# Optimization experiments

Hardware: AMD Instinct MI355X
Metric: run time of the kernel (lower is better)

## Reference

```python
import jax, jax.numpy as jnp
import numpy as np

B, N, C = 1, 768, 128


def _safe_cdist(x):
    # Euclidean pairwise distance, grad-safe at zero (diagonal).
    sq = jnp.sum(x * x, axis=-1)  # (b, n)
    d2 = sq[:, :, None] + sq[:, None, :] - 2.0 * jnp.einsum('bmi,bni->bmn', x, x)
    d2 = jnp.maximum(d2, 0.0)
    pos = d2 > 0
    return jnp.where(pos, jnp.sqrt(jnp.where(pos, d2, 1.0)), 0.0)


def _bilinear(h, Wa, ba, Wb, bb):
    # Gated bilinear unit: Linear_a(h) * Linear_b(h)
    return (h @ Wa.T + ba) * (h @ Wb.T + bb)


def setup_inputs() -> dict:
    key = jax.random.key(0)
    ks = jax.random.split(key, 16)
    x = jax.random.normal(ks[0], (B, N, 3), dtype=jnp.float32)

    def lin(k, fan_in, fan_out):
        k1, k2 = jax.random.split(k)
        s = 1.0 / np.sqrt(fan_in)
        W = jax.random.uniform(k1, (fan_out, fan_in), jnp.float32, -s, s)
        b = jax.random.uniform(k2, (fan_out,), jnp.float32, -s, s)
        return W, b

    Wa1, ba1 = lin(ks[1], 3, C)
    Wb1, bb1 = lin(ks[2], 3, C)
    Wa2, ba2 = lin(ks[3], C, C)
    Wb2, bb2 = lin(ks[4], C, C)
    Wa3, ba3 = lin(ks[5], C, C)
    Wb3, bb3 = lin(ks[6], C, C)
    Wf, _ = lin(ks[7], C, 2)  # final bias unused by the einsum in forward
    return {"x": x,
            "Wa1": Wa1, "ba1": ba1, "Wb1": Wb1, "bb1": bb1,
            "Wa2": Wa2, "ba2": ba2, "Wb2": Wb2, "bb2": bb2,
            "Wa3": Wa3, "ba3": ba3, "Wb3": Wb3, "bb3": bb3,
            "Wf": Wf}


def reference(x, Wa1, ba1, Wb1, bb1, Wa2, ba2, Wb2, bb2, Wa3, ba3, Wb3, bb3, Wf):
    b, n, _ = x.shape
    nrm = jnp.linalg.norm(x, axis=-1, keepdims=True)          # (b, n, 1)
    nrm_m = jnp.broadcast_to(nrm, (b, n, n))                  # row norms
    d = _safe_cdist(x)                                        # (b, n, n)
    h = jnp.stack([d, nrm_m, jnp.swapaxes(nrm_m, 1, 2)], axis=-1)  # (b,n,n,3)
    h = _bilinear(h, Wa1, ba1, Wb1, bb1)
    h = _bilinear(h, Wa2, ba2, Wb2, bb2)
    h = _bilinear(h, Wa3, ba3, Wb3, bb3)                      # (b,n,n,C)
    att = jax.nn.softmax(h, axis=-2)                          # softmax over n (dim=-2)
    # einsum('bmnc,bni->bmic') followed by sum over m, fused:
    agg = jnp.einsum('bmnc,bni->bic', att, x)                 # (b, 3, C)
    agg = jnp.swapaxes(agg, 1, 2)                             # (b, C, 3)
    out = jnp.einsum('bnd,on->bod', agg, Wf)                  # (b, 2, 3)
    return jnp.concatenate([x[:, :1], out[:, :2]], axis=1)    # (b, 3, 3)
```

## Files before the change

### kernel.cpp

```cpp
#include <hip/hip_runtime.h>

#define NPTS 768
#define CCH  128
#define NM4  36
#define NM2  10
#define NCHUNK 2
#define CTILE (NPTS/NCHUNK)
#define PAIR (NPTS*CCH)
#define NACC 384
#define FINB 96
#define LOG2E 1.4426950408889634f

typedef __attribute__((ext_vector_type(8))) short bf16x8;
typedef __attribute__((ext_vector_type(16))) float f32x16;
union Frag { unsigned int u[4]; bf16x8 h; };

__device__ __forceinline__ float fast_exp2(float x) {
  return __builtin_amdgcn_exp2f(x);
}

__device__ __forceinline__ void split3(float x, unsigned int& h0,
                                       unsigned int& h1, unsigned int& h2) {
  const unsigned int b0 = __float_as_uint(x);
  h0 = b0 >> 16;
  const float r1 = x - __uint_as_float(b0 & 0xFFFF0000u);
  const unsigned int b1 = __float_as_uint(r1);
  h1 = b1 >> 16;
  const float r2 = r1 - __uint_as_float(b1 & 0xFFFF0000u);
  h2 = __float_as_uint(r2) >> 16;
}

__device__ __forceinline__ int t4i(int a, int b, int c) {
  int t = 0;
  for (int aa = 0; aa < a; ++aa) t += (5 - aa) * (6 - aa) / 2;
  for (int bb = 0; bb < b; ++bb) t += (5 - a - bb);
  return t + c;
}
__device__ __forceinline__ int t2i(int a, int b, int c) {
  int t = 0;
  for (int aa = 0; aa < a; ++aa) t += (3 - aa) * (4 - aa) / 2;
  for (int bb = 0; bb < b; ++bb) t += (3 - a - bb);
  return t + c;
}

__global__ __launch_bounds__(128) void k_fold12(
    const float* __restrict__ x,
    const float* __restrict__ Wa1, const float* __restrict__ ba1,
    const float* __restrict__ Wb1, const float* __restrict__ bb1,
    const float* __restrict__ Wa2, const float* __restrict__ ba2,
    const float* __restrict__ Wb2, const float* __restrict__ bb2,
    float* __restrict__ norms, float* __restrict__ C2m,
    float* __restrict__ apart, unsigned int* __restrict__ ticket) {
  __shared__ float sA[128][NM2];
  __shared__ float sB[128][NM2];
  const int c = blockIdx.x;
  const int k = threadIdx.x;

  if (c < 6) {
    const int i = c*128 + k;
    const float p0 = x[3*i], p1 = x[3*i+1], p2 = x[3*i+2];
    norms[i] = sqrtf(p0*p0 + p1*p1 + p2*p2);
  }
  if (c == 6) {
    apart[k] = 0.f; apart[CCH + k] = 0.f; apart[2*CCH + k] = 0.f;
    if (k == 0) *ticket = 0u;
  }

  {
    const float A0 = Wa1[3*k], A1 = Wa1[3*k+1], A2c = Wa1[3*k+2], A3 = ba1[k];
    const float B0 = Wb1[3*k], B1 = Wb1[3*k+1], B2c = Wb1[3*k+2], B3 = bb1[k];
    const float g0 = A3*B3;
    const float g1 = A2c*B3 + A3*B2c;
    const float g2 = A2c*B2c;
    const float g3 = A1*B3 + A3*B1;
    const float g4 = A1*B2c + A2c*B1;
    const float g5 = A1*B1;
    const float g6 = A0*B3 + A3*B0;
    const float g7 = A0*B2c + A2c*B0;
    const float g8 = A0*B1 + A1*B0;
    const float g9 = A0*B0;
    const float wa = Wa2[c*CCH + k];
    const float wb = Wb2[c*CCH + k];
    sA[k][0] = wa*g0; sB[k][0] = wb*g0;
    sA[k][1] = wa*g1; sB[k][1] = wb*g1;
    sA[k][2] = wa*g2; sB[k][2] = wb*g2;
    sA[k][3] = wa*g3; sB[k][3] = wb*g3;
    sA[k][4] = wa*g4; sB[k][4] = wb*g4;
    sA[k][5] = wa*g5; sB[k][5] = wb*g5;
    sA[k][6] = wa*g6; sB[k][6] = wb*g6;
    sA[k][7] = wa*g7; sB[k][7] = wb*g7;
    sA[k][8] = wa*g8; sB[k][8] = wb*g8;
    sA[k][9] = wa*g9; sB[k][9] = wb*g9;
  }
  __syncthreads();

  for (int s = 64; s >= 1; s >>= 1) {
    if (k < s) {
      for (int t = 0; t < NM2; ++t) {
        sA[k][t] += sA[k+s][t];
        sB[k][t] += sB[k+s][t];
      }
    }
    __syncthreads();
  }
  if (k == 0) {
    sA[0][0] += ba2[c];
    sB[0][0] += bb2[c];
  }
  __syncthreads();

  if (k < 35) {
    int rem = k, a = 0;
    while (rem >= (5 - a)*(6 - a)/2) { rem -= (5 - a)*(6 - a)/2; ++a; }
    int b = 0;
    while (rem >= 5 - a - b) { rem -= 5 - a - b; ++b; }
    const int cc = rem;
    float s = 0.f;
    const int deg = a + b + cc;
    for (int a1 = 0; a1 <= a && a1 <= 2; ++a1)
      for (int b1 = 0; b1 <= b && b1 <= 2; ++b1)
        for (int c1 = 0; c1 <= cc && c1 <= 2; ++c1) {
          const int d1 = a1 + b1 + c1;
          if (d1 <= 2 && (deg - d1) <= 2)
            s += sA[0][t2i(a1, b1, c1)]
               * sB[0][t2i(a - a1, b - b1, cc - c1)];
        }
    C2m[c*NM4 + k] = s;
  }
  if (k == 35) C2m[c*NM4 + 35] = 0.f;
}

__global__ void k_pre2(const float* __restrict__ Wa3, const float* __restrict__ ba3,
                       const float* __restrict__ Wb3, const float* __restrict__ bb3,
                       const float* __restrict__ C2m,
                       float* __restrict__ A3mT, float* __restrict__ B3mT) {
  const int c = blockIdx.x;
  const int j = threadIdx.x;
  if (j >= NM4) return;
  float sa = 0.f, sb = 0.f;
  if (j < 35) {
    for (int k = 0; k < CCH; ++k) {
      const float v = C2m[k*NM4 + j];
      sa += Wa3[c*CCH + k] * v;
      sb += Wb3[c*CCH + k] * v;
    }
    if (j == 0) { sa += ba3[c]; sb += bb3[c]; }
  }
  A3mT[j*CCH + c] = sa;
  B3mT[j*CCH + c] = sb;
}

__global__ __launch_bounds__(256, 4) void k_main(
    const float* __restrict__ x, const float* __restrict__ norms,
    const float* __restrict__ A3mT, const float* __restrict__ B3mT,
    float* __restrict__ Mp, float* __restrict__ Sp,
    float* __restrict__ A0p, float* __restrict__ A1p, float* __restrict__ A2p) {
  __shared__ __align__(16) float4 xt[CTILE];
  const int tid = threadIdx.x;
  const int wid = tid >> 6;
  const int lane = tid & 63;
  const int hl = lane >> 5;
  const int ln = lane & 31;
  const int m = blockIdx.x;
  const int chunk = blockIdx.y;
  const int c = wid*32 + ln;

  for (int p = tid; p < CTILE; p += 256) {
    const int n = chunk*CTILE + p;
    xt[p] = make_float4(x[3*n], x[3*n+1], x[3*n+2], norms[n]);
  }

  const float u = norms[m];
  const float xm0 = x[3*m], xm1 = x[3*m+1], xm2 = x[3*m+2];
  const float uu = u*u;
  const float up[5] = {1.f, u, uu, uu*u, uu*uu};

  Frag ba0, ba1, ba2, bb0, bb1, bb2;
  #pragma unroll
  for (int p = 0; p < 4; ++p) {
    unsigned int wa0 = 0, wa1 = 0, wa2 = 0, wb0 = 0, wb1 = 0, wb2 = 0;
    #pragma unroll
    for (int half = 0; half < 2; ++half) {
      const int t = 8*hl + 2*p + half;
      int rem = t, i = 0;
      while (i < 5 && rem >= 5 - i) { rem -= 5 - i; ++i; }
      const int j = rem;
      float sa = 0.f, sb = 0.f;
      #pragma unroll
      for (int b = 0; b < 5; ++b) {
        if (i + j + b <= 4) {
          const int idx = t4i(i, b, j)*CCH + c;
          sa = fmaf(A3mT[idx], up[b], sa);
          sb = fmaf(B3mT[idx], up[b], sb);
        }
      }
      sa *= LOG2E;
      unsigned int a0, a1, a2, b0, b1, b2;
      split3(sa, a0, a1, a2);
      split3(sb, b0, b1, b2);
      const int sh = half*16;
      wa0 |= a0 << sh; wa1 |= a1 << sh; wa2 |= a2 << sh;
      wb0 |= b0 << sh; wb1 |= b1 << sh; wb2 |= b2 << sh;
    }
    ba0.u[p] = wa0; ba1.u[p] = wa1; ba2.u[p] = wa2;
    bb0.u[p] = wb0; bb1.u[p] = wb1; bb2.u[p] = wb2;
  }

  __syncthreads();

  float mrun = -INFINITY, srun = 0.f, a0r = 0.f, a1r = 0.f, a2r = 0.f;

  for (int tile = 0; tile < CTILE/32; ++tile) {
    const float4 xn = xt[tile*32 + ln];
    const float v = xn.w;
    const float dot = xm0*xn.x + xm1*xn.y + xm2*xn.z;
    const float d2 = uu + v*v - 2.f*dot;
    const float d = (d2 > 0.f) ? sqrtf(d2) : 0.f;
    const float v2 = v*v, v3 = v2*v, v4 = v2*v2;
    const float dd = d*d, d3 = dd*d, d4 = dd*dd;
    float mono[8];
    if (hl == 0) {
      mono[0] = 1.f;   mono[1] = v;     mono[2] = v2;    mono[3] = v3;
      mono[4] = v4;    mono[5] = d;     mono[6] = d*v;   mono[7] = d*v2;
    } else {
      mono[0] = d*v3;  mono[1] = dd;    mono[2] = dd*v;  mono[3] = dd*v2;
      mono[4] = d3;    mono[5] = d3*v;  mono[6] = d4;    mono[7] = 0.f;
    }
    Frag A0f, A1f, A2f;
    #pragma unroll
    for (int p = 0; p < 4; ++p) {
      unsigned int l0, l1, l2, g0, g1, g2;
      split3(mono[2*p],   l0, l1, l2);
      split3(mono[2*p+1], g0, g1, g2);
      A0f.u[p] = l0 | (g0 << 16);
      A1f.u[p] = l1 | (g1 << 16);
      A2f.u[p] = l2 | (g2 << 16);
    }

    f32x16 accA, accB;
    #pragma unroll
    for (int r = 0; r < 16; ++r) { accA[r] = 0.f; accB[r] = 0.f; }
    accA = __builtin_amdgcn_mfma_f32_32x32x16_bf16(A2f.h, ba0.h, accA, 0, 0, 0);
    accA = __builtin_amdgcn_mfma_f32_32x32x16_bf16(A1f.h, ba1.h, accA, 0, 0, 0);
    accA = __builtin_amdgcn_mfma_f32_32x32x16_bf16(A0f.h, ba2.h, accA, 0, 0, 0);
    accA = __builtin_amdgcn_mfma_f32_32x32x16_bf16(A1f.h, ba0.h, accA, 0, 0, 0);
    accA = __builtin_amdgcn_mfma_f32_32x32x16_bf16(A0f.h, ba1.h, accA, 0, 0, 0);
    accA = __builtin_amdgcn_mfma_f32_32x32x16_bf16(A0f.h, ba0.h, accA, 0, 0, 0);
    accB = __builtin_amdgcn_mfma_f32_32x32x16_bf16(A2f.h, bb0.h, accB, 0, 0, 0);
    accB = __builtin_amdgcn_mfma_f32_32x32x16_bf16(A1f.h, bb1.h, accB, 0, 0, 0);
    accB = __builtin_amdgcn_mfma_f32_32x32x16_bf16(A0f.h, bb2.h, accB, 0, 0, 0);
    accB = __builtin_amdgcn_mfma_f32_32x32x16_bf16(A1f.h, bb0.h, accB, 0, 0, 0);
    accB = __builtin_amdgcn_mfma_f32_32x32x16_bf16(A0f.h, bb1.h, accB, 0, 0, 0);
    accB = __builtin_amdgcn_mfma_f32_32x32x16_bf16(A0f.h, bb0.h, accB, 0, 0, 0);

    float hv[16];
    #pragma unroll
    for (int r = 0; r < 16; ++r) hv[r] = accA[r]*accB[r];
    float hx = hv[0];
    #pragma unroll
    for (int r = 1; r < 16; ++r) hx = fmaxf(hx, hv[r]);
    const float mnew = fmaxf(mrun, hx);
    const float sc = fast_exp2(mrun - mnew);
    mrun = mnew;
    float s_ = srun*sc, A0_ = a0r*sc, A1_ = a1r*sc, A2_ = a2r*sc;
    #pragma unroll
    for (int rg = 0; rg < 4; ++rg) {
      #pragma unroll
      for (int q = 0; q < 4; ++q) {
        const float e = fast_exp2(hv[rg*4 + q] - mnew);
        const float4 xv = xt[tile*32 + rg*8 + hl*4 + q];
        s_ += e;
        A0_ = fmaf(e, xv.x, A0_);
        A1_ = fmaf(e, xv.y, A1_);
        A2_ = fmaf(e, xv.z, A2_);
      }
    }
    srun = s_; a0r = A0_; a1r = A1_; a2r = A2_;
  }

  {
    const float om = __shfl_xor(mrun, 32);
    const float os = __shfl_xor(srun, 32);
    const float o0 = __shfl_xor(a0r, 32);
    const float o1 = __shfl_xor(a1r, 32);
    const float o2 = __shfl_xor(a2r, 32);
    const float M  = fmaxf(mrun, om);
    const float e1 = fast_exp2(mrun - M);
    const float e2 = fast_exp2(om - M);
    if (hl == 0) {
      const int idx = chunk*PAIR + m*CCH + c;
      Mp[idx]  = M;
      Sp[idx]  = fmaf(srun, e1, os*e2);
      A0p[idx] = fmaf(a0r, e1, o0*e2);
      A1p[idx] = fmaf(a1r, e1, o1*e2);
      A2p[idx] = fmaf(a2r, e1, o2*e2);
    }
  }
}

__global__ __launch_bounds__(256) void k_fin(
    const float* __restrict__ x,
    const float* __restrict__ Mp, const float* __restrict__ Sp,
    const float* __restrict__ A0p, const float* __restrict__ A1p,
    const float* __restrict__ A2p,
    const float* __restrict__ Wf,
    float* __restrict__ apart, unsigned int* __restrict__ ticket,
    float* __restrict__ out) {
  __shared__ float red2[2][3][CCH];
  __shared__ float red[CCH][6];
  __shared__ bool last;
  const int tid = threadIdx.x;
  const int ml = tid >> 7;
  const int c = tid & 127;

  float s0 = 0.f, s1 = 0.f, s2 = 0.f;
  #pragma unroll
  for (int j = 0; j < 4; ++j) {
    const int m = blockIdx.x*8 + ml*4 + j;
    const int gid = m*CCH + c;
    const float m0 = Mp[0*PAIR + gid], m1 = Mp[1*PAIR + gid];
    const float M = fmaxf(m0, m1);
    const float e0 = fast_exp2(m0 - M), e1 = fast_exp2(m1 - M);
    const float W  = Sp[0*PAIR+gid]*e0 + Sp[1*PAIR+gid]*e1;
    const float g0 = A0p[0*PAIR+gid]*e0 + A0p[1*PAIR+gid]*e1;
    const float g1 = A1p[0*PAIR+gid]*e0 + A1p[1*PAIR+gid]*e1;
    const float g2 = A2p[0*PAIR+gid]*e0 + A2p[1*PAIR+gid]*e1;
    const float inv = 1.f / W;
    s0 = fmaf(g0, inv, s0);
    s1 = fmaf(g1, inv, s1);
    s2 = fmaf(g2, inv, s2);
  }
  red2[ml][0][c] = s0; red2[ml][1][c] = s1; red2[ml][2][c] = s2;
  __syncthreads();
  for (int p = tid; p < NACC; p += 256) {
    const int i = p >> 7, cc = p & 127;
    atomicAdd(&apart[p], red2[0][i][cc] + red2[1][i][cc]);
  }
  __threadfence();
  __syncthreads();
  if (tid == 0) {
    const unsigned int old = atomicAdd(ticket, 1u);
    last = (old == FINB - 1);
  }
  __syncthreads();
  if (!last) return;
  __threadfence();

  if (tid < CCH) {
    const int cc = tid;
    const float a0 = __hip_atomic_load(&apart[cc],          __ATOMIC_RELAXED, __HIP_MEMORY_SCOPE_AGENT);
    const float a1 = __hip_atomic_load(&apart[CCH + cc],    __ATOMIC_RELAXED, __HIP_MEMORY_SCOPE_AGENT);
    const float a2 = __hip_atomic_load(&apart[2*CCH + cc],  __ATOMIC_RELAXED, __HIP_MEMORY_SCOPE_AGENT);
    const float w0 = Wf[cc], w1 = Wf[CCH + cc];
    red[cc][0] = w0*a0; red[cc][1] = w0*a1; red[cc][2] = w0*a2;
    red[cc][3] = w1*a0; red[cc][4] = w1*a1; red[cc][5] = w1*a2;
  }
  __syncthreads();
  if (tid < 6) {
    float s = 0.f;
    for (int k = 0; k < CCH; ++k) s += red[k][tid];
    out[3 + tid] = s;
  }
  if (tid < 3) out[tid] = x[tid];
}

extern "C" void kernel_launch(void* const* d_in, const int* in_sizes, int n_in,
                              void* d_out, int out_size, void* d_ws, size_t ws_size,
                              hipStream_t stream) {
  const float* x   = (const float*)d_in[0];
  const float* Wa1 = (const float*)d_in[1];
  const float* ba1 = (const float*)d_in[2];
  const float* Wb1 = (const float*)d_in[3];
  const float* bb1 = (const float*)d_in[4];
  const float* Wa2 = (const float*)d_in[5];
  const float* ba2 = (const float*)d_in[6];
  const float* Wb2 = (const float*)d_in[7];
  const float* bb2 = (const float*)d_in[8];
  const float* Wa3 = (const float*)d_in[9];
  const float* ba3 = (const float*)d_in[10];
  const float* Wb3 = (const float*)d_in[11];
  const float* bb3 = (const float*)d_in[12];
  const float* Wf  = (const float*)d_in[13];
  float* out = (float*)d_out;

  float* ws     = (float*)d_ws;
  float* norms  = ws;
  float* C2m    = norms + NPTS;
  float* A3mT   = C2m   + CCH*NM4;
  float* B3mT   = A3mT  + NM4*CCH;
  float* Mp     = B3mT  + NM4*CCH;
  float* Sp     = Mp    + NCHUNK*PAIR;
  float* A0p    = Sp    + NCHUNK*PAIR;
  float* A1p    = A0p   + NCHUNK*PAIR;
  float* A2p    = A1p   + NCHUNK*PAIR;
  float* apart  = A2p   + NCHUNK*PAIR;
  unsigned int* ticket = (unsigned int*)(apart + NACC);

  hipLaunchKernelGGL(k_fold12, dim3(CCH), dim3(128), 0, stream,
                     x, Wa1, ba1, Wb1, bb1, Wa2, ba2, Wb2, bb2,
                     norms, C2m, apart, ticket);
  hipLaunchKernelGGL(k_pre2, dim3(CCH), dim3(64), 0, stream,
                     Wa3, ba3, Wb3, bb3, C2m, A3mT, B3mT);
  hipLaunchKernelGGL(k_main, dim3(NPTS, NCHUNK), dim3(256), 0, stream,
                     x, norms, A3mT, B3mT, Mp, Sp, A0p, A1p, A2p);
  hipLaunchKernelGGL(k_fin, dim3(FINB), dim3(256), 0, stream,
                     x, Mp, Sp, A0p, A1p, A2p, Wf, apart, ticket, out);
}
```

Measured before the change: 155.7 us.

## Split softmax columns into four chunks and streamline online softmax update

Raises the column chunk count from 2 to 4, which doubles the grid of the main kernel, and raises the occupancy hint to 6 blocks per SM. The per-thread weight fold now uses compile-time templated indices, and the tile loop is fully unrolled. The online softmax fuses the product with the max subtraction and only rescales the accumulators when the running max grows. The reduction kernel is generalised to merge NCHUNK partials, so it now reads twice as much partial data and adds more writes to global memory.

After: 393.1 us. 152% more time.

```diff
diff --git a/kernel.cpp b/kernel.cpp
--- a/kernel.cpp
+++ b/kernel.cpp
@@ -4,8 +4,9 @@
 #define CCH  128
 #define NM4  36
 #define NM2  10
-#define NCHUNK 2
+#define NCHUNK 4
 #define CTILE (NPTS/NCHUNK)
+#define NT   (CTILE/32)
 #define PAIR (NPTS*CCH)
 #define NACC 384
 #define FINB 96
@@ -30,7 +31,7 @@
   h2 = __float_as_uint(r2) >> 16;
 }
 
-__device__ __forceinline__ int t4i(int a, int b, int c) {
+__device__ constexpr int ct4i(int a, int b, int c) {
   int t = 0;
   for (int aa = 0; aa < a; ++aa) t += (5 - aa) * (6 - aa) / 2;
   for (int bb = 0; bb < b; ++bb) t += (5 - a - bb);
@@ -41,6 +42,47 @@
   for (int aa = 0; aa < a; ++aa) t += (3 - aa) * (4 - aa) / 2;
   for (int bb = 0; bb < b; ++bb) t += (3 - a - bb);
   return t + c;
+}
+__device__ constexpr int tdi(int t) { return t<5?0 : t<9?1 : t<12?2 : t<14?3 : 4; }
+__device__ constexpr int tdj(int t) { return t<5?t : t<9?t-5 : t<12?t-9 : t<14?t-12 : 0; }
+
+template<int T>
+__device__ __forceinline__ void fold_one(const float* __restrict__ A3,
+                                         const float* __restrict__ B3, int c,
+                                         float u1, float u2, float u3, float u4,
+                                         float& sa, float& sb) {
+  if constexpr (T >= 15) { sa = 0.f; sb = 0.f; }
+  else {
+    constexpr int I = tdi(T), J = tdj(T);
+    sa = A3[ct4i(I,0,J)*CCH + c];
+    sb = B3[ct4i(I,0,J)*CCH + c];
+    if constexpr (I+J+1 <= 4) { sa = fmaf(A3[ct4i(I,1,J)*CCH+c], u1, sa);
+                                sb = fmaf(B3[ct4i(I,1,J)*CCH+c], u1, sb); }
+    if constexpr (I+J+2 <= 4) { sa = fmaf(A3[ct4i(I,2,J)*CCH+c], u2, sa);
+                                sb = fmaf(B3[ct4i(I,2,J)*CCH+c], u2, sb); }
+    if constexpr (I+J+3 <= 4) { sa = fmaf(A3[ct4i(I,3,J)*CCH+c], u3, sa);
+                                sb = fmaf(B3[ct4i(I,3,J)*CCH+c], u3, sb); }
+    if constexpr (I+J+4 <= 4) { sa = fmaf(A3[ct4i(I,4,J)*CCH+c], u4, sa);
+                                sb = fmaf(B3[ct4i(I,4,J)*CCH+c], u4, sb); }
+  }
+}
+
+template<int TLO, int THI>
+__device__ __forceinline__ void fold_word(const float* __restrict__ A3,
+                                          const float* __restrict__ B3, int c,
+                                          float u1, float u2, float u3, float u4,
+                                          unsigned int& wa0, unsigned int& wa1,
+                                          unsigned int& wa2, unsigned int& wb0,
+                                          unsigned int& wb1, unsigned int& wb2) {
+  float salo, sblo, sahi, sbhi;
+  fold_one<TLO>(A3, B3, c, u1, u2, u3, u4, salo, sblo);
+  fold_one<THI>(A3, B3, c, u1, u2, u3, u4, sahi, sbhi);
+  salo *= LOG2E; sahi *= LOG2E;
+  unsigned int a0,a1,a2, c0,c1,c2, b0,b1,b2, d0,d1,d2;
+  split3(salo, a0, a1, a2); split3(sahi, c0, c1, c2);
+  split3(sblo, b0, b1, b2); split3(sbhi, d0, d1, d2);
+  wa0 = a0 | (c0 << 16); wa1 = a1 | (c1 << 16); wa2 = a2 | (c2 << 16);
+  wb0 = b0 | (d0 << 16); wb1 = b1 | (d1 << 16); wb2 = b2 | (d2 << 16);
 }
 
 __global__ __launch_bounds__(128) void k_fold12(
@@ -150,7 +192,7 @@
   B3mT[j*CCH + c] = sb;
 }
 
-__global__ __launch_bounds__(256, 4) void k_main(
+__global__ __launch_bounds__(256, 6) void k_main(
     const float* __restrict__ x, const float* __restrict__ norms,
     const float* __restrict__ A3mT, const float* __restrict__ B3mT,
     float* __restrict__ Mp, float* __restrict__ Sp,
@@ -173,44 +215,27 @@
   const float u = norms[m];
   const float xm0 = x[3*m], xm1 = x[3*m+1], xm2 = x[3*m+2];
   const float uu = u*u;
-  const float up[5] = {1.f, u, uu, uu*u, uu*uu};
+  const float u1 = u, u2 = uu, u3 = uu*u, u4 = uu*uu;
 
   Frag ba0, ba1, ba2, bb0, bb1, bb2;
+  if (hl == 0) {
+    fold_word<0,1>(A3mT, B3mT, c, u1,u2,u3,u4, ba0.u[0],ba1.u[0],ba2.u[0], bb0.u[0],bb1.u[0],bb2.u[0]);
+    fold_word<2,3>(A3mT, B3mT, c, u1,u2,u3,u4, ba0.u[1],ba1.u[1],ba2.u[1], bb0.u[1],bb1.u[1],bb2.u[1]);
+    fold_word<4,5>(A3mT, B3mT, c, u1,u2,u3,u4, ba0.u[2],ba1.u[2],ba2.u[2], bb0.u[2],bb1.u[2],bb2.u[2]);
+    fold_word<6,7>(A3mT, B3mT, c, u1,u2,u3,u4, ba0.u[3],ba1.u[3],ba2.u[3], bb0.u[3],bb1.u[3],bb2.u[3]);
+  } else {
+    fold_word<8,9>  (A3mT, B3mT, c, u1,u2,u3,u4, ba0.u[0],ba1.u[0],ba2.u[0], bb0.u[0],bb1.u[0],bb2.u[0]);
+    fold_word<10,11>(A3mT, B3mT, c, u1,u2,u3,u4, ba0.u[1],ba1.u[1],ba2.u[1], bb0.u[1],bb1.u[1],bb2.u[1]);
+    fold_word<12,13>(A3mT, B3mT, c, u1,u2,u3,u4, ba0.u[2],ba1.u[2],ba2.u[2], bb0.u[2],bb1.u[2],bb2.u[2]);
+    fold_word<14,15>(A3mT, B3mT, c, u1,u2,u3,u4, ba0.u[3],ba1.u[3],ba2.u[3], bb0.u[3],bb1.u[3],bb2.u[3]);
+  }
+
+  __syncthreads();
+
+  float mrun = -INFINITY, srun = 0.f, a0r = 0.f, a1r = 0.f, a2r = 0.f;
+
   #pragma unroll
-  for (int p = 0; p < 4; ++p) {
-    unsigned int wa0 = 0, wa1 = 0, wa2 = 0, wb0 = 0, wb1 = 0, wb2 = 0;
-    #pragma unroll
-    for (int half = 0; half < 2; ++half) {
-      const int t = 8*hl + 2*p + half;
-      int rem = t, i = 0;
-      while (i < 5 && rem >= 5 - i) { rem -= 5 - i; ++i; }
-      const int j = rem;
-      float sa = 0.f, sb = 0.f;
-      #pragma unroll
-      for (int b = 0; b < 5; ++b) {
-        if (i + j + b <= 4) {
-          const int idx = t4i(i, b, j)*CCH + c;
-          sa = fmaf(A3mT[idx], up[b], sa);
-          sb = fmaf(B3mT[idx], up[b], sb);
-        }
-      }
-      sa *= LOG2E;
-      unsigned int a0, a1, a2, b0, b1, b2;
-      split3(sa, a0, a1, a2);
-      split3(sb, b0, b1, b2);
-      const int sh = half*16;
-      wa0 |= a0 << sh; wa1 |= a1 << sh; wa2 |= a2 << sh;
-      wb0 |= b0 << sh; wb1 |= b1 << sh; wb2 |= b2 << sh;
-    }
-    ba0.u[p] = wa0; ba1.u[p] = wa1; ba2.u[p] = wa2;
-    bb0.u[p] = wb0; bb1.u[p] = wb1; bb2.u[p] = wb2;
-  }
-
-  __syncthreads();
-
-  float mrun = -INFINITY, srun = 0.f, a0r = 0.f, a1r = 0.f, a2r = 0.f;
-
-  for (int tile = 0; tile < CTILE/32; ++tile) {
+  for (int tile = 0; tile < NT; ++tile) {
     const float4 xn = xt[tile*32 + ln];
     const float v = xn.w;
     const float dot = xm0*xn.x + xm1*xn.y + xm2*xn.z;
@@ -253,29 +278,57 @@
     accB = __builtin_amdgcn_mfma_f32_32x32x16_bf16(A0f.h, bb1.h, accB, 0, 0, 0);
     accB = __builtin_amdgcn_mfma_f32_32x32x16_bf16(A0f.h, bb0.h, accB, 0, 0, 0);
 
-    float hv[16];
-    #pragma unroll
-    for (int r = 0; r < 16; ++r) hv[r] = accA[r]*accB[r];
-    float hx = hv[0];
-    #pragma unroll
-    for (int r = 1; r < 16; ++r) hx = fmaxf(hx, hv[r]);
-    const float mnew = fmaxf(mrun, hx);
-    const float sc = fast_exp2(mrun - mnew);
-    mrun = mnew;
-    float s_ = srun*sc, A0_ = a0r*sc, A1_ = a1r*sc, A2_ = a2r*sc;
+    float e[16];
+    if (tile == 0) {
+      float hv[16];
+      #pragma unroll
+      for (int r = 0; r < 16; ++r) hv[r] = accA[r]*accB[r];
+      const float x0 = fmaxf(fmaxf(hv[0], hv[1]), hv[2]);
+      const float x1 = fmaxf(fmaxf(hv[3], hv[4]), hv[5]);
+      const float x2 = fmaxf(fmaxf(hv[6], hv[7]), hv[8]);
+      const float x3 = fmaxf(fmaxf(hv[9], hv[10]), hv[11]);
+      const float x4 = fmaxf(fmaxf(hv[12], hv[13]), hv[14]);
+      const float y0 = fmaxf(fmaxf(x0, x1), x2);
+      const float y1 = fmaxf(fmaxf(x3, x4), hv[15]);
+      mrun = fmaxf(y0, y1);
+      #pragma unroll
+      for (int r = 0; r < 16; ++r) e[r] = fast_exp2(hv[r] - mrun);
+    } else {
+      float f[16];
+      #pragma unroll
+      for (int r = 0; r < 16; ++r) f[r] = fmaf(accA[r], accB[r], -mrun);
+      const float x0 = fmaxf(fmaxf(f[0], f[1]), f[2]);
+      const float x1 = fmaxf(fmaxf(f[3], f[4]), f[5]);
+      const float x2 = fmaxf(fmaxf(f[6], f[7]), f[8]);
+      const float x3 = fmaxf(fmaxf(f[9], f[10]), f[11]);
+      const float x4 = fmaxf(fmaxf(f[12], f[13]), f[14]);
+      const float y0 = fmaxf(fmaxf(x0, x1), x2);
+      const float y1 = fmaxf(fmaxf(x3, x4), f[15]);
+      const float fx = fmaxf(y0, y1);
+      if (fx > 0.f) {
+        const float sc = fast_exp2(-fx);
+        srun *= sc; a0r *= sc; a1r *= sc; a2r *= sc;
+        mrun += fx;
+        #pragma unroll
+        for (int r = 0; r < 16; ++r) e[r] = fast_exp2(f[r] - fx);
+      } else {
+        #pragma unroll
+        for (int r = 0; r < 16; ++r) e[r] = fast_exp2(f[r]);
+      }
+    }
+
     #pragma unroll
     for (int rg = 0; rg < 4; ++rg) {
       #pragma unroll
       for (int q = 0; q < 4; ++q) {
-        const float e = fast_exp2(hv[rg*4 + q] - mnew);
+        const float ee = e[rg*4 + q];
         const float4 xv = xt[tile*32 + rg*8 + hl*4 + q];
-        s_ += e;
-        A0_ = fmaf(e, xv.x, A0_);
-        A1_ = fmaf(e, xv.y, A1_);
-        A2_ = fmaf(e, xv.z, A2_);
+        srun += ee;
+        a0r = fmaf(ee, xv.x, a0r);
+        a1r = fmaf(ee, xv.y, a1r);
+        a2r = fmaf(ee, xv.z, a2r);
       }
     }
-    srun = s_; a0r = A0_; a1r = A1_; a2r = A2_;
   }
 
   {
@@ -318,13 +371,21 @@
   for (int j = 0; j < 4; ++j) {
     const int m = blockIdx.x*8 + ml*4 + j;
     const int gid = m*CCH + c;
-    const float m0 = Mp[0*PAIR + gid], m1 = Mp[1*PAIR + gid];
-    const float M = fmaxf(m0, m1);
-    const float e0 = fast_exp2(m0 - M), e1 = fast_exp2(m1 - M);
-    const float W  = Sp[0*PAIR+gid]*e0 + Sp[1*PAIR+gid]*e1;
-    const float g0 = A0p[0*PAIR+gid]*e0 + A0p[1*PAIR+gid]*e1;
-    const float g1 = A1p[0*PAIR+gid]*e0 + A1p[1*PAIR+gid]*e1;
-    const float g2 = A2p[0*PAIR+gid]*e0 + A2p[1*PAIR+gid]*e1;
+    float mm[NCHUNK];
+    #pragma unroll
+    for (int p = 0; p < NCHUNK; ++p) mm[p] = Mp[p*PAIR + gid];
+    float M = mm[0];
+    #pragma unroll
+    for (int p = 1; p < NCHUNK; ++p) M = fmaxf(M, mm[p]);
+    float W = 0.f, g0 = 0.f, g1 = 0.f, g2 = 0.f;
+    #pragma unroll
+    for (int p = 0; p < NCHUNK; ++p) {
+      const float ep = fast_exp2(mm[p] - M);
+      W  = fmaf(Sp[p*PAIR+gid],  ep, W);
+      g0 = fmaf(A0p[p*PAIR+gid], ep, g0);
+      g1 = fmaf(A1p[p*PAIR+gid], ep, g1);
+      g2 = fmaf(A2p[p*PAIR+gid], ep, g2);
+    }
     const float inv = 1.f / W;
     s0 = fmaf(g0, inv, s0);
     s1 = fmaf(g1, inv, s1);
```
